# Kernel optimization log

Hardware: AMD Instinct MI355X
Metric: run time of the kernel (lower is better)

## Reference

```python
import jax, jax.numpy as jnp
import numpy as np
import math

B, S, D_MODEL, HEADS, GRID = 4, 2048, 512, 8, 8
HEAD_DIM = D_MODEL // HEADS
A_C, K_C, C_C = 0.9724108095811765, 0.9884401790754128, 0.999449553483052


def setup_inputs() -> dict:
    key = jax.random.key(0)
    ks = jax.random.split(key, 4)
    q = jax.random.normal(ks[0], (B, S, D_MODEL), jnp.float32)
    mask = jnp.tril(jnp.ones((S, S), dtype=bool))[None, None]  # causal (1,1,S,S)
    out_dim = 3 * D_MODEL
    grid_norm = jnp.arange(1, GRID + 1, dtype=jnp.float32)  # (grid,)
    # is_first=True init: normal(0,0.4)/output_dim/grid_norm_factor
    amplitudes = jax.random.normal(ks[1], (out_dim, D_MODEL, GRID), jnp.float32) * 0.4 / out_dim / grid_norm
    # norm_freq with is_first=True -> freq = arange(1..grid) / (grid+1)**0 = arange
    freq = jnp.arange(1, GRID + 1, dtype=jnp.float32)  # (grid,)
    grid_phase = jnp.arange(1, GRID + 1, dtype=jnp.float32) / (GRID + 1)
    input_phase = jnp.linspace(0.0, math.pi, D_MODEL, dtype=jnp.float32)[:, None]  # (in,1)
    phase0 = grid_phase[None, :] + input_phase  # (in, grid)
    ratio = 1.0
    for i in range(1, GRID):
        ratio *= A_C * i ** (-K_C) + C_C
    phase = phase0 * np.float32(ratio)
    kan_bias = jnp.ones((out_dim,), jnp.float32) / out_dim
    lim = math.sqrt(6.0 / (D_MODEL + D_MODEL))  # xavier_uniform
    out_w = jax.random.uniform(ks[2], (D_MODEL, D_MODEL), jnp.float32, -lim, lim)
    out_b = jnp.zeros((D_MODEL,), jnp.float32)
    return {"q": q, "mask": mask, "freq": freq, "phase": phase,
            "amplitudes": amplitudes, "kan_bias": kan_bias,
            "out_w": out_w, "out_b": out_b}


def sinekan(x2d, freq, phase, amp, bias):
    # y[n,j] = sum_{k,l} sin(x[n,k]*f[l] + p[k,l]) * amp[j,k,l] + bias[j]
    # expand sin(a+p) = sin(a)cos(p) + cos(a)sin(p); fold phase into weights
    ang = x2d[:, :, None] * freq  # (N, in, grid)
    w_sin = amp * jnp.cos(phase)  # (out, in, grid)
    w_cos = amp * jnp.sin(phase)
    y = (jnp.einsum('nkl,jkl->nj', jnp.sin(ang), w_sin)
         + jnp.einsum('nkl,jkl->nj', jnp.cos(ang), w_cos))
    return y + bias


def rotate_half(u):
    u1, u2 = jnp.split(u, 2, axis=-1)
    return jnp.concatenate([-u2, u1], axis=-1)


def apply_rope(x, pos_emb):
    cos, sin = jnp.split(pos_emb, 2, axis=-1)  # each (S, head_dim//2)
    x_even, x_odd = x[..., ::2], x[..., 1::2]
    x1 = x_even * cos + rotate_half(x_odd) * sin
    x2 = x_odd * cos + rotate_half(x_even) * sin
    return jnp.concatenate([x1, x2], axis=-1)


def rope_emb(seq_len, dim):
    half = dim // 2
    inv_freq = 1.0 / (10000.0 ** (jnp.arange(half, dtype=jnp.float32) / half))
    ang = jnp.arange(seq_len, dtype=jnp.float32)[:, None] * inv_freq  # (S, half)
    return jnp.concatenate([jnp.cos(ang), jnp.sin(ang)], axis=-1)  # (S, dim)


def reference(q, mask, freq, phase, amplitudes, kan_bias, out_w, out_b):
    b, s, _ = q.shape
    qkv = sinekan(q.reshape(-1, D_MODEL), freq, phase, amplitudes, kan_bias)
    qkv = qkv.reshape(b, s, HEADS, 3 * HEAD_DIM).transpose(0, 2, 1, 3)  # (b,h,s,3d)
    qs, ks, vs = jnp.split(qkv, 3, axis=-1)
    pe = rope_emb(s, HEAD_DIM)
    qs = apply_rope(qs, pe)
    ks = apply_rope(ks, pe)
    scores = jnp.einsum('bhqd,bhkd->bhqk', qs, ks) / math.sqrt(HEAD_DIM)
    scores = jnp.where(mask, scores.astype(jnp.float32), -1e9)
    attn = jax.nn.softmax(scores, axis=-1)
    ctx = jnp.einsum('bhqk,bhkd->bhqd', attn, vs)
    ctx = ctx.transpose(0, 2, 1, 3).reshape(b, s, D_MODEL)
    return ctx @ out_w.T + out_b
```

## Files before the change

kernel.cpp:

```cpp
#include <hip/hip_runtime.h>
#include <math.h>


typedef __attribute__((ext_vector_type(8))) short bf16x8;
typedef __attribute__((ext_vector_type(8))) unsigned short ushort8;
typedef __attribute__((ext_vector_type(4))) unsigned short ushort4v;
typedef __attribute__((ext_vector_type(4))) float f32x4;

#define DEV __device__ __forceinline__

DEV unsigned short f2bf(float f) {
  unsigned u = __builtin_bit_cast(unsigned, f);
  u += 0x7FFFu + ((u >> 16) & 1u);
  return (unsigned short)(u >> 16);
}
DEV float bf2f(unsigned short h) {
  unsigned u = ((unsigned)h) << 16;
  return __builtin_bit_cast(float, u);
}

#define GLDS16(gp, lp)                                                         \
  __builtin_amdgcn_global_load_lds(                                            \
      (const __attribute__((address_space(1))) void*)(gp),                     \
      (__attribute__((address_space(3))) void*)(lp), 16, 0, 0)

__global__ __launch_bounds__(256) void wprep(const float* __restrict__ amp,
                                             const float* __restrict__ phase,
                                             unsigned short* __restrict__ Wb) {
  int id = blockIdx.x * 256 + threadIdx.x;
  int j = id >> 9;
  int k = id & 511;
  const float* ap = amp + (size_t)id * 8;
  const float* ph = phase + k * 8;
  union { unsigned short u[16]; uint4 v[2]; } pk;
#pragma unroll
  for (int l = 0; l < 8; ++l) {
    float sp, cp;
    sincosf(ph[l], &sp, &cp);
    float a = ap[l];
    pk.u[l] = f2bf(a * cp);
    pk.u[8 + l] = f2bf(a * sp);
  }
  uint4* dst = (uint4*)(Wb + (size_t)j * 8192 + k * 16);
  dst[0] = pk.v[0];
  dst[1] = pk.v[1];
}

__global__ __launch_bounds__(256) void owprep(const float* __restrict__ w,
                                              unsigned short* __restrict__ o) {
  int id = blockIdx.x * 256 + threadIdx.x;
  o[id] = f2bf(w[id]);
}

__global__ __launch_bounds__(256) void fgen(const float* __restrict__ q,
                                            unsigned short* __restrict__ F) {
  int id = blockIdx.x * 256 + threadIdx.x;
  int row = id >> 9;
  int dim = id & 511;
  float x = q[(size_t)row * 512 + dim];
  union { unsigned short u[16]; uint4 v[2]; } fr;
#pragma unroll
  for (int l = 1; l <= 8; ++l) {
    float a = x * (float)l;
    fr.u[l - 1] = f2bf(__sinf(a));
    fr.u[7 + l] = f2bf(__cosf(a));
  }
  uint4* dst = (uint4*)(F + (size_t)row * 8192 + dim * 16);
  dst[0] = fr.v[0];
  dst[1] = fr.v[1];
}

__global__ __launch_bounds__(512, 2) void kan_gemm8(
    const unsigned short* __restrict__ F, const unsigned short* __restrict__ Wb,
    const float* __restrict__ bias, unsigned short* __restrict__ qkv) {
  __shared__ __align__(16) char LDS[114688];

  const int tid = threadIdx.x, lane = tid & 63, wid = tid >> 6;
  const int wm = wid >> 2, wn = wid & 3;
  const int l15 = lane & 15, kg = lane >> 4;

  int bid = blockIdx.x;
  int xcd = bid & 7, u = bid >> 3;
  const int m0 = (xcd * 4 + (u & 3)) * 256;
  const int n0 = (u >> 2) * 192;

  const int growl = wid * 8 + (lane >> 3);
  const int cswz = ((lane & 7) ^ (lane >> 3)) << 4;

  f32x4 acc[2][4][3] = {};
  bf16x8 af[4][2], bf[3][2];

#define STAGE_A(T, C)                                                           \
  GLDS16((const char*)F + (size_t)(m0 + (C)*64 + growl) * 16384 +               \
             (size_t)(T) * 128 + cswz,                                          \
         LDS + (((T)&1) * 32768 + (C)*8192 + wid * 1024))

#define STAGE_B(T, C)                                                           \
  GLDS16((const char*)Wb + (size_t)(n0 + (C)*64 + growl) * 16384 +              \
             (size_t)(T) * 128 + cswz,                                          \
         LDS + (65536 + ((T)&1) * 24576 + (C)*8192 + wid * 1024))

#define DSREAD_A(T, MQ)                                                         \
  do {                                                                          \
    _Pragma("unroll") for (int mi = 0; mi < 4; ++mi)                            \
        _Pragma("unroll") for (int kk = 0; kk < 2; ++kk) {                      \
      int _r = (MQ)*128 + wm * 64 + mi * 16 + l15;                              \
      af[mi][kk] = *(const bf16x8*)(LDS + ((T)&1) * 32768 + _r * 128 +          \
                                    (((kk * 4 + kg) ^ (l15 & 7)) << 4));        \
    }                                                                           \
  } while (0)

#define DSREAD_B(T)                                                             \
  do {                                                                          \
    _Pragma("unroll") for (int ni = 0; ni < 3; ++ni)                            \
        _Pragma("unroll") for (int kk = 0; kk < 2; ++kk) {                      \
      int _r = wn * 48 + ni * 16 + l15;                                         \
      bf[ni][kk] = *(const bf16x8*)(LDS + 65536 + ((T)&1) * 24576 + _r * 128 +  \
                                    (((kk * 4 + kg) ^ (l15 & 7)) << 4));        \
    }                                                                           \
  } while (0)

#define MFMAS(MQ, NI0, NI1)                                                     \
  do {                                                                          \
    __builtin_amdgcn_s_setprio(1);                                              \
    _Pragma("unroll") for (int mi = 0; mi < 4; ++mi)                            \
        _Pragma("unroll") for (int ni = (NI0); ni <= (NI1); ++ni)               \
            _Pragma("unroll") for (int kk = 0; kk < 2; ++kk)                    \
                acc[MQ][mi][ni] = __builtin_amdgcn_mfma_f32_16x16x32_bf16(      \
                    af[mi][kk], bf[ni][kk], acc[MQ][mi][ni], 0, 0, 0);          \
    __builtin_amdgcn_s_setprio(0);                                              \
  } while (0)

#define BAR __builtin_amdgcn_s_barrier()
#define VMW(N) asm volatile("s_waitcnt vmcnt(" #N ")" ::: "memory")
#define LGW                                                                     \
  do {                                                                          \
    asm volatile("s_waitcnt lgkmcnt(0)" ::: "memory");                          \
    __builtin_amdgcn_sched_barrier(0);                                          \
  } while (0)

  STAGE_A(0, 0); STAGE_A(0, 1);
  STAGE_B(0, 0); STAGE_B(0, 1); STAGE_B(0, 2);
  STAGE_A(0, 2); STAGE_A(0, 3);

#pragma unroll 2
  for (int t = 0; t < 127; ++t) {
    VMW(2); BAR;
    DSREAD_A(t, 0); DSREAD_B(t);
    STAGE_A(t + 1, 0); STAGE_A(t + 1, 1);
    LGW; MFMAS(0, 0, 1);
    BAR;
    STAGE_B(t + 1, 0); STAGE_B(t + 1, 1);
    MFMAS(0, 2, 2);
    VMW(4); BAR;
    DSREAD_A(t, 1);
    STAGE_B(t + 1, 2); STAGE_A(t + 1, 2);
    LGW; MFMAS(1, 0, 1);
    BAR;
    STAGE_A(t + 1, 3);
    MFMAS(1, 2, 2);
  }
  {
    const int t = 127;
    VMW(2); BAR;
    DSREAD_A(t, 0); DSREAD_B(t);
    LGW; MFMAS(0, 0, 1);
    BAR;
    MFMAS(0, 2, 2);
    VMW(0); BAR;
    DSREAD_A(t, 1);
    LGW; MFMAS(1, 0, 1);
    BAR;
    MFMAS(1, 2, 2);
  }

#pragma unroll
  for (int mq = 0; mq < 2; ++mq)
#pragma unroll
    for (int mi = 0; mi < 4; ++mi)
#pragma unroll
      for (int ni = 0; ni < 3; ++ni) {
        int row = m0 + mq * 128 + wm * 64 + mi * 16 + kg * 4;
        int col = n0 + wn * 48 + ni * 16 + l15;
        float bv = bias[col];
        f32x4 a = acc[mq][mi][ni];
#pragma unroll
        for (int j = 0; j < 4; ++j)
          qkv[(size_t)(row + j) * 1536 + col] = f2bf(a[j] + bv);
      }
#undef STAGE_A
#undef STAGE_B
#undef DSREAD_A
#undef DSREAD_B
#undef MFMAS
#undef BAR
#undef VMW
#undef LGW
}

__global__ __launch_bounds__(256) void rope_prep(const unsigned short* __restrict__ qkv,
                                                 unsigned short* __restrict__ Qr,
                                                 unsigned short* __restrict__ Kr) {
  int id = blockIdx.x * 256 + threadIdx.x;
  int i = id & 31;
  int row = id >> 5;
  int s = row & 2047;
  int bh = row >> 11;
  int b = bh >> 3, h = bh & 7;

  const unsigned short* base = qkv + ((size_t)(b * 2048 + s)) * 1536 + h * 192;

  float inv = exp2f(-(float)i * (13.287712379549449f / 32.0f));
  float ang = (float)s * inv;
  float sn, cs;
  sincosf(ang, &sn, &cs);

  int pi = (i < 16) ? i + 16 : i - 16;
  float sign = (i < 16) ? -1.f : 1.f;
  size_t orow = (size_t)row * 64;

  {
    const unsigned short* xp = base;
    float xe = bf2f(xp[2 * i]), xo = bf2f(xp[2 * i + 1]);
    float po = bf2f(xp[2 * pi + 1]), pe = bf2f(xp[2 * pi]);
    Qr[orow + i] = f2bf(xe * cs + sign * po * sn);
    Qr[orow + 32 + i] = f2bf(xo * cs + sign * pe * sn);
  }
  {
    const unsigned short* xp = base + 64;
    float xe = bf2f(xp[2 * i]), xo = bf2f(xp[2 * i + 1]);
    float po = bf2f(xp[2 * pi + 1]), pe = bf2f(xp[2 * pi]);
    Kr[orow + i] = f2bf(xe * cs + sign * po * sn);
    Kr[orow + 32 + i] = f2bf(xo * cs + sign * pe * sn);
  }
}

__global__ __launch_bounds__(256) void attn(const unsigned short* __restrict__ Qr,
                                            const unsigned short* __restrict__ Kr,
                                            const unsigned short* __restrict__ qkv,
                                            unsigned short* __restrict__ ctx) {
  __shared__ __align__(16) unsigned short Klds[32 * 64];
  __shared__ __align__(16) unsigned short Vt[64 * 36];
  __shared__ __align__(16) unsigned short Plds[4 * 512];

  const int tid = threadIdx.x;
  const int lane = tid & 63;
  const int w = tid >> 6;
  const int qb = blockIdx.x;
  const int bh = blockIdx.y;
  const int b = bh >> 3, h = bh & 7;
  const int qw = qb * 64 + w * 16;
  const int l15 = lane & 15, kg = lane >> 4;

  const unsigned short* Qp = Qr + ((size_t)bh * 2048 + qw + l15) * 64 + kg * 8;
  bf16x8 qf0 = *(const bf16x8*)Qp;
  bf16x8 qf1 = *(const bf16x8*)(Qp + 32);

  f32x4 octx[4] = {};
  float den[4] = {0.f, 0.f, 0.f, 0.f};
  unsigned short* Pw = &Plds[w * 512];

  const int skp = tid >> 3;
  const int sds = tid & 7;
  const int vd = tid & 63;
  const int vkq = tid >> 6;

  const int nkt = 2 * qb + 2;
  for (int kt = 0; kt < nkt; ++kt) {
    ushort8 kv =
        *(const ushort8*)(Kr + ((size_t)bh * 2048 + kt * 32 + skp) * 64 + sds * 8);
    *(ushort8*)((char*)Klds + ((skp * 128 + sds * 16) ^ ((skp & 7) << 4))) = kv;
    {
      const unsigned short* vcol = qkv +
          ((size_t)(b * 2048 + kt * 32 + vkq * 8)) * 1536 + h * 192 + 128 + vd;
      ushort4v lo, hi;
      lo.x = vcol[0];
      lo.y = vcol[1536];
      lo.z = vcol[2 * 1536];
      lo.w = vcol[3 * 1536];
      hi.x = vcol[4 * 1536];
      hi.y = vcol[5 * 1536];
      hi.z = vcol[6 * 1536];
      hi.w = vcol[7 * 1536];
      *(ushort4v*)&Vt[vd * 36 + vkq * 8] = lo;
      *(ushort4v*)&Vt[vd * 36 + vkq * 8 + 4] = hi;
    }
    __syncthreads();

    f32x4 zero = {0.f, 0.f, 0.f, 0.f};
#pragma unroll
    for (int f = 0; f < 2; ++f) {
      int kp = f * 16 + l15;
      int swk = (kp & 7) << 4;
      bf16x8 kf0 = *(const bf16x8*)((char*)Klds + ((kp * 128 + kg * 16) ^ swk));
      bf16x8 kf1 = *(const bf16x8*)((char*)Klds + ((kp * 128 + 64 + kg * 16) ^ swk));
      f32x4 sA = __builtin_amdgcn_mfma_f32_16x16x32_bf16(qf0, kf0, zero, 0, 0, 0);
      sA = __builtin_amdgcn_mfma_f32_16x16x32_bf16(qf1, kf1, sA, 0, 0, 0);
      int kgl = kt * 32 + kp;
#pragma unroll
      for (int j = 0; j < 4; ++j) {
        int qrow = qw + kg * 4 + j;
        float p = (kgl <= qrow) ? __expf(sA[j] * 0.125f) : 0.f;
        den[j] += p;
        int prow = kg * 4 + j;
        *(unsigned short*)((char*)Pw +
                           ((prow * 64 + kp * 2) ^ ((prow & 3) << 4))) = f2bf(p);
      }
    }
    bf16x8 pf =
        *(const bf16x8*)((char*)Pw + ((l15 * 64 + kg * 16) ^ ((l15 & 3) << 4)));
#pragma unroll
    for (int nd = 0; nd < 4; ++nd) {
      int d = nd * 16 + l15;
      union { ushort4v h[2]; bf16x8 v; } vfu;
      vfu.h[0] = *(const ushort4v*)&Vt[d * 36 + kg * 8];
      vfu.h[1] = *(const ushort4v*)&Vt[d * 36 + kg * 8 + 4];
      octx[nd] = __builtin_amdgcn_mfma_f32_16x16x32_bf16(pf, vfu.v, octx[nd], 0, 0, 0);
    }
    __syncthreads();
  }

#pragma unroll
  for (int j = 0; j < 4; ++j) {
    float d_ = den[j];
    d_ += __shfl_xor(d_, 1);
    d_ += __shfl_xor(d_, 2);
    d_ += __shfl_xor(d_, 4);
    d_ += __shfl_xor(d_, 8);
    den[j] = d_;
  }
#pragma unroll
  for (int nd = 0; nd < 4; ++nd)
#pragma unroll
    for (int j = 0; j < 4; ++j) {
      int qrow = qw + kg * 4 + j;
      int col = h * 64 + nd * 16 + l15;
      ctx[((size_t)b * 2048 + qrow) * 512 + col] = f2bf(octx[nd][j] / den[j]);
    }
}

__global__ __launch_bounds__(256) void out_gemm(const unsigned short* __restrict__ A,
                                                const unsigned short* __restrict__ Bw,
                                                const float* __restrict__ outb,
                                                float* __restrict__ out) {
  __shared__ __align__(16) unsigned short Al[128 * 32];
  __shared__ __align__(16) unsigned short Bl[128 * 32];
  const int tid = threadIdx.x, lane = tid & 63, w = tid >> 6;
  const int wm = w >> 1, wn = w & 1;
  const int m0 = blockIdx.x * 128, n0 = blockIdx.y * 128;
  const int l15 = lane & 15, kg = lane >> 4;

  f32x4 acc[4][4] = {};

  const unsigned short* ga = A + (size_t)(m0 + (tid >> 2)) * 512 + (tid & 3) * 8;
  const unsigned short* gb = Bw + (size_t)(n0 + (tid >> 2)) * 512 + (tid & 3) * 8;

  for (int t = 0; t < 16; ++t) {
    GLDS16(ga + t * 32, &Al[w * 512]);
    GLDS16(ga + t * 32 + 64 * 512, &Al[2048 + w * 512]);
    GLDS16(gb + t * 32, &Bl[w * 512]);
    GLDS16(gb + t * 32 + 64 * 512, &Bl[2048 + w * 512]);
    __syncthreads();

    bf16x8 af[4], bfr[4];
#pragma unroll
    for (int m = 0; m < 4; ++m)
      af[m] = *(const bf16x8*)&Al[(wm * 64 + m * 16 + l15) * 32 + kg * 8];
#pragma unroll
    for (int n = 0; n < 4; ++n)
      bfr[n] = *(const bf16x8*)&Bl[(wn * 64 + n * 16 + l15) * 32 + kg * 8];
#pragma unroll
    for (int m = 0; m < 4; ++m)
#pragma unroll
      for (int n = 0; n < 4; ++n)
        acc[m][n] =
            __builtin_amdgcn_mfma_f32_16x16x32_bf16(af[m], bfr[n], acc[m][n], 0, 0, 0);

    __syncthreads();
  }

  const int rb = m0 + wm * 64 + kg * 4;
  const int cb = n0 + wn * 64 + l15;
#pragma unroll
  for (int n = 0; n < 4; ++n) {
    int cc = cb + n * 16;
    float bv = outb[cc];
#pragma unroll
    for (int m = 0; m < 4; ++m)
#pragma unroll
      for (int j = 0; j < 4; ++j)
        out[(size_t)(rb + m * 16 + j) * 512 + cc] = acc[m][n][j] + bv;
  }
}

extern "C" void kernel_launch(void* const* d_in, const int* in_sizes, int n_in,
                              void* d_out, int out_size, void* d_ws, size_t ws_size,
                              hipStream_t stream) {
  const float* q = (const float*)d_in[0];
  const float* phase = (const float*)d_in[3];
  const float* amp = (const float*)d_in[4];
  const float* kbias = (const float*)d_in[5];
  const float* out_w = (const float*)d_in[6];
  const float* out_b = (const float*)d_in[7];
  float* out = (float*)d_out;

  char* p = (char*)d_ws;
  unsigned short* Wb = (unsigned short*)(p);
  unsigned short* qkv = (unsigned short*)(p + 25165824);
  unsigned short* Qr = (unsigned short*)(p + 50331648);
  unsigned short* Kr = (unsigned short*)(p + 58720256);
  unsigned short* ctx = (unsigned short*)(p + 67108864);
  unsigned short* Wob = (unsigned short*)(p + 75497472);
  unsigned short* F = (unsigned short*)(p + 76021760);

  owprep<<<1024, 256, 0, stream>>>(out_w, Wob);
  wprep<<<3072, 256, 0, stream>>>(amp, phase, Wb);
  fgen<<<16384, 256, 0, stream>>>(q, F);
  kan_gemm8<<<256, 512, 0, stream>>>(F, Wb, kbias, qkv);
  rope_prep<<<8192, 256, 0, stream>>>(qkv, Qr, Kr);
  attn<<<dim3(32, 32), 256, 0, stream>>>(Qr, Kr, qkv, ctx);
  out_gemm<<<dim3(64, 4), 256, 0, stream>>>(ctx, Wob, out_b, out);
}
```

Baseline: 319.9 us.

## Use angle-addition sincos in fgen, prefetch A in GEMM, enlarge attention tiles

fgen now calls sincosf once and builds the harmonics 2..8 with the angle-addition recurrence instead of eight sin/cos pairs, cutting transcendental work at some cost in accuracy. The KAN GEMM double-buffers its A fragments so the second-half LDS reads are issued earlier, overlapping them with MFMAs and removing one lgkm wait. The attention kernel moves to 512 threads with 128 query rows and 64-key tiles per block, loads V with a swizzled 16-byte LDS store, and uses a padded P layout. This halves the number of attention blocks and the per-key-tile sync overhead.

Measured after the change: 303.2 us. 5.2% less time.

```diff
diff --git a/kernel.cpp b/kernel.cpp
--- a/kernel.cpp
+++ b/kernel.cpp
@@ -4,7 +4,6 @@
 
 typedef __attribute__((ext_vector_type(8))) short bf16x8;
 typedef __attribute__((ext_vector_type(8))) unsigned short ushort8;
-typedef __attribute__((ext_vector_type(4))) unsigned short ushort4v;
 typedef __attribute__((ext_vector_type(4))) float f32x4;
 
 #define DEV __device__ __forceinline__
@@ -58,12 +57,19 @@
   int row = id >> 9;
   int dim = id & 511;
   float x = q[(size_t)row * 512 + dim];
+  float s1, c1;
+  sincosf(x, &s1, &c1);
   union { unsigned short u[16]; uint4 v[2]; } fr;
-#pragma unroll
-  for (int l = 1; l <= 8; ++l) {
-    float a = x * (float)l;
-    fr.u[l - 1] = f2bf(__sinf(a));
-    fr.u[7 + l] = f2bf(__cosf(a));
+  float s = s1, c = c1;
+  fr.u[0] = f2bf(s);
+  fr.u[8] = f2bf(c);
+#pragma unroll
+  for (int l = 1; l < 8; ++l) {
+    float ns = s * c1 + c * s1;
+    float nc = c * c1 - s * s1;
+    s = ns; c = nc;
+    fr.u[l] = f2bf(s);
+    fr.u[8 + l] = f2bf(c);
   }
   uint4* dst = (uint4*)(F + (size_t)row * 8192 + dim * 16);
   dst[0] = fr.v[0];
@@ -88,7 +94,7 @@
   const int cswz = ((lane & 7) ^ (lane >> 3)) << 4;
 
   f32x4 acc[2][4][3] = {};
-  bf16x8 af[4][2], bf[3][2];
+  bf16x8 af0[4][2], af1[4][2], bf[3][2];
 
 #define STAGE_A(T, C)                                                           \
   GLDS16((const char*)F + (size_t)(m0 + (C)*64 + growl) * 16384 +               \
@@ -100,13 +106,13 @@
              (size_t)(T) * 128 + cswz,                                          \
          LDS + (65536 + ((T)&1) * 24576 + (C)*8192 + wid * 1024))
 
-#define DSREAD_A(T, MQ)                                                         \
+#define DSREAD_A(DST, T, MQ)                                                    \
   do {                                                                          \
     _Pragma("unroll") for (int mi = 0; mi < 4; ++mi)                            \
         _Pragma("unroll") for (int kk = 0; kk < 2; ++kk) {                      \
       int _r = (MQ)*128 + wm * 64 + mi * 16 + l15;                              \
-      af[mi][kk] = *(const bf16x8*)(LDS + ((T)&1) * 32768 + _r * 128 +          \
-                                    (((kk * 4 + kg) ^ (l15 & 7)) << 4));        \
+      DST[mi][kk] = *(const bf16x8*)(LDS + ((T)&1) * 32768 + _r * 128 +         \
+                                     (((kk * 4 + kg) ^ (l15 & 7)) << 4));       \
     }                                                                           \
   } while (0)
 
@@ -120,14 +126,14 @@
     }                                                                           \
   } while (0)
 
-#define MFMAS(MQ, NI0, NI1)                                                     \
+#define MFMAS(AF, MQ, NI0, NI1)                                                 \
   do {                                                                          \
     __builtin_amdgcn_s_setprio(1);                                              \
     _Pragma("unroll") for (int mi = 0; mi < 4; ++mi)                            \
         _Pragma("unroll") for (int ni = (NI0); ni <= (NI1); ++ni)               \
             _Pragma("unroll") for (int kk = 0; kk < 2; ++kk)                    \
                 acc[MQ][mi][ni] = __builtin_amdgcn_mfma_f32_16x16x32_bf16(      \
-                    af[mi][kk], bf[ni][kk], acc[MQ][mi][ni], 0, 0, 0);          \
+                    AF[mi][kk], bf[ni][kk], acc[MQ][mi][ni], 0, 0, 0);          \
     __builtin_amdgcn_s_setprio(0);                                              \
   } while (0)
 
@@ -146,32 +152,32 @@
 #pragma unroll 2
   for (int t = 0; t < 127; ++t) {
     VMW(2); BAR;
-    DSREAD_A(t, 0); DSREAD_B(t);
+    DSREAD_A(af0, t, 0); DSREAD_B(t);
     STAGE_A(t + 1, 0); STAGE_A(t + 1, 1);
-    LGW; MFMAS(0, 0, 1);
+    LGW; MFMAS(af0, 0, 0, 1);
     BAR;
+    DSREAD_A(af1, t, 1);
     STAGE_B(t + 1, 0); STAGE_B(t + 1, 1);
-    MFMAS(0, 2, 2);
+    MFMAS(af0, 0, 2, 2);
     VMW(4); BAR;
-    DSREAD_A(t, 1);
     STAGE_B(t + 1, 2); STAGE_A(t + 1, 2);
-    LGW; MFMAS(1, 0, 1);
+    MFMAS(af1, 1, 0, 1);
     BAR;
     STAGE_A(t + 1, 3);
-    MFMAS(1, 2, 2);
+    MFMAS(af1, 1, 2, 2);
   }
   {
     const int t = 127;
     VMW(2); BAR;
-    DSREAD_A(t, 0); DSREAD_B(t);
-    LGW; MFMAS(0, 0, 1);
+    DSREAD_A(af0, t, 0); DSREAD_B(t);
+    LGW; MFMAS(af0, 0, 0, 1);
     BAR;
-    MFMAS(0, 2, 2);
+    DSREAD_A(af1, t, 1);
+    MFMAS(af0, 0, 2, 2);
     VMW(0); BAR;
-    DSREAD_A(t, 1);
-    LGW; MFMAS(1, 0, 1);
+    MFMAS(af1, 1, 0, 1);
     BAR;
-    MFMAS(1, 2, 2);
+    MFMAS(af1, 1, 2, 2);
   }
 
 #pragma unroll
@@ -235,13 +241,13 @@
   }
 }
 
-__global__ __launch_bounds__(256) void attn(const unsigned short* __restrict__ Qr,
+__global__ __launch_bounds__(512) void attn(const unsigned short* __restrict__ Qr,
                                             const unsigned short* __restrict__ Kr,
                                             const unsigned short* __restrict__ qkv,
                                             unsigned short* __restrict__ ctx) {
-  __shared__ __align__(16) unsigned short Klds[32 * 64];
-  __shared__ __align__(16) unsigned short Vt[64 * 36];
-  __shared__ __align__(16) unsigned short Plds[4 * 512];
+  __shared__ __align__(16) char KB[8192];
+  __shared__ __align__(16) char VT[8192];
+  __shared__ __align__(16) char PL[18432];
 
   const int tid = threadIdx.x;
   const int lane = tid & 63;
@@ -249,7 +255,7 @@
   const int qb = blockIdx.x;
   const int bh = blockIdx.y;
   const int b = bh >> 3, h = bh & 7;
-  const int qw = qb * 64 + w * 16;
+  const int qw = qb * 128 + w * 16;
   const int l15 = lane & 15, kg = lane >> 4;
 
   const unsigned short* Qp = Qr + ((size_t)bh * 2048 + qw + l15) * 64 + kg * 8;
@@ -258,7 +264,7 @@
 
   f32x4 octx[4] = {};
   float den[4] = {0.f, 0.f, 0.f, 0.f};
-  unsigned short* Pw = &Plds[w * 512];
+  char* Pw = PL + w * 2304;
 
   const int skp = tid >> 3;
   const int sds = tid & 7;
@@ -268,54 +274,47 @@
   const int nkt = 2 * qb + 2;
   for (int kt = 0; kt < nkt; ++kt) {
     ushort8 kv =
-        *(const ushort8*)(Kr + ((size_t)bh * 2048 + kt * 32 + skp) * 64 + sds * 8);
-    *(ushort8*)((char*)Klds + ((skp * 128 + sds * 16) ^ ((skp & 7) << 4))) = kv;
+        *(const ushort8*)(Kr + ((size_t)bh * 2048 + kt * 64 + skp) * 64 + sds * 8);
+    *(ushort8*)(KB + ((skp * 128 + sds * 16) ^ ((skp & 7) << 4))) = kv;
     {
-      const unsigned short* vcol = qkv +
-          ((size_t)(b * 2048 + kt * 32 + vkq * 8)) * 1536 + h * 192 + 128 + vd;
-      ushort4v lo, hi;
-      lo.x = vcol[0];
-      lo.y = vcol[1536];
-      lo.z = vcol[2 * 1536];
-      lo.w = vcol[3 * 1536];
-      hi.x = vcol[4 * 1536];
-      hi.y = vcol[5 * 1536];
-      hi.z = vcol[6 * 1536];
-      hi.w = vcol[7 * 1536];
-      *(ushort4v*)&Vt[vd * 36 + vkq * 8] = lo;
-      *(ushort4v*)&Vt[vd * 36 + vkq * 8 + 4] = hi;
+      const unsigned short* vcol =
+          qkv + ((size_t)(b * 2048 + kt * 64 + vkq * 8)) * 1536 + h * 192 + 128 + vd;
+      ushort8 vv;
+#pragma unroll
+      for (int jj = 0; jj < 8; ++jj) vv[jj] = vcol[jj * 1536];
+      *(ushort8*)(VT + (vd * 128 + ((vkq * 16) ^ ((vd & 7) << 4)))) = vv;
     }
     __syncthreads();
 
     f32x4 zero = {0.f, 0.f, 0.f, 0.f};
 #pragma unroll
-    for (int f = 0; f < 2; ++f) {
+    for (int f = 0; f < 4; ++f) {
       int kp = f * 16 + l15;
       int swk = (kp & 7) << 4;
-      bf16x8 kf0 = *(const bf16x8*)((char*)Klds + ((kp * 128 + kg * 16) ^ swk));
-      bf16x8 kf1 = *(const bf16x8*)((char*)Klds + ((kp * 128 + 64 + kg * 16) ^ swk));
+      bf16x8 kf0 = *(const bf16x8*)(KB + ((kp * 128 + kg * 16) ^ swk));
+      bf16x8 kf1 = *(const bf16x8*)(KB + ((kp * 128 + 64 + kg * 16) ^ swk));
       f32x4 sA = __builtin_amdgcn_mfma_f32_16x16x32_bf16(qf0, kf0, zero, 0, 0, 0);
       sA = __builtin_amdgcn_mfma_f32_16x16x32_bf16(qf1, kf1, sA, 0, 0, 0);
-      int kgl = kt * 32 + kp;
+      int kgl = kt * 64 + kp;
 #pragma unroll
       for (int j = 0; j < 4; ++j) {
         int qrow = qw + kg * 4 + j;
         float p = (kgl <= qrow) ? __expf(sA[j] * 0.125f) : 0.f;
         den[j] += p;
         int prow = kg * 4 + j;
-        *(unsigned short*)((char*)Pw +
-                           ((prow * 64 + kp * 2) ^ ((prow & 3) << 4))) = f2bf(p);
+        *(unsigned short*)(Pw + prow * 144 + kp * 2) = f2bf(p);
       }
     }
-    bf16x8 pf =
-        *(const bf16x8*)((char*)Pw + ((l15 * 64 + kg * 16) ^ ((l15 & 3) << 4)));
+    bf16x8 pf0 = *(const bf16x8*)(Pw + l15 * 144 + kg * 16);
+    bf16x8 pf1 = *(const bf16x8*)(Pw + l15 * 144 + 64 + kg * 16);
 #pragma unroll
     for (int nd = 0; nd < 4; ++nd) {
       int d = nd * 16 + l15;
-      union { ushort4v h[2]; bf16x8 v; } vfu;
-      vfu.h[0] = *(const ushort4v*)&Vt[d * 36 + kg * 8];
-      vfu.h[1] = *(const ushort4v*)&Vt[d * 36 + kg * 8 + 4];
-      octx[nd] = __builtin_amdgcn_mfma_f32_16x16x32_bf16(pf, vfu.v, octx[nd], 0, 0, 0);
+      int swv = (d & 7) << 4;
+      bf16x8 vf0 = *(const bf16x8*)(VT + (d * 128 + ((kg * 16) ^ swv)));
+      bf16x8 vf1 = *(const bf16x8*)(VT + (d * 128 + ((64 + kg * 16) ^ swv)));
+      octx[nd] = __builtin_amdgcn_mfma_f32_16x16x32_bf16(pf0, vf0, octx[nd], 0, 0, 0);
+      octx[nd] = __builtin_amdgcn_mfma_f32_16x16x32_bf16(pf1, vf1, octx[nd], 0, 0, 0);
     }
     __syncthreads();
   }
@@ -418,6 +417,6 @@
   fgen<<<16384, 256, 0, stream>>>(q, F);
   kan_gemm8<<<256, 512, 0, stream>>>(F, Wb, kbias, qkv);
   rope_prep<<<8192, 256, 0, stream>>>(qkv, Qr, Kr);
-  attn<<<dim3(32, 32), 256, 0, stream>>>(Qr, Kr, qkv, ctx);
+  attn<<<dim3(16, 32), 512, 0, stream>>>(Qr, Kr, qkv, ctx);
   out_gemm<<<dim3(64, 4), 256, 0, stream>>>(ctx, Wob, out_b, out);
 }
```
